# Performance work log

Hardware: AMD Instinct MI355X
Metric: run time of the kernel (lower is better)

## Reference

```python
import jax, jax.numpy as jnp
import numpy as np

BN_EPS = 1e-5


def _gcn_norm(edge_index, n):
    # PyG gcn_norm with add_self_loops=True: deg counts in-degree incl. self loop
    loops = jnp.arange(n, dtype=edge_index.dtype)
    src = jnp.concatenate([edge_index[0], loops])
    dst = jnp.concatenate([edge_index[1], loops])
    deg = jax.ops.segment_sum(jnp.ones(src.shape[0], jnp.float32), dst, num_segments=n)
    dinv = jnp.where(deg > 0, jax.lax.rsqrt(jnp.maximum(deg, 1.0)), 0.0)
    norm = dinv[src] * dinv[dst]  # [E + N]
    return src, dst, norm


def _gcn_conv(x, src, dst, norm, W, b, n):
    h = x @ W                      # dense transform first (fewer FLOPs: d_out gather)
    msgs = h[src] * norm[:, None]  # [E+N, d_out] gathered, degree-normalized
    return jax.ops.segment_sum(msgs, dst, num_segments=n) + b


def _bn_relu(x, gamma, beta):
    # BatchNorm1d in training mode: biased batch stats over node dim
    mu = x.mean(axis=0)
    var = x.var(axis=0)
    return jax.nn.relu(gamma * (x - mu) * jax.lax.rsqrt(var + BN_EPS) + beta)


def setup_inputs() -> dict:
    key = jax.random.key(0)
    ks = jax.random.split(key, 8)
    N, E, D_IN, H1, H2, D_OUT = 50000, 500000, 128, 256, 512, 128
    x = jax.random.normal(ks[0], (N, D_IN), jnp.float32)
    edge_index = jax.random.randint(ks[1], (2, E), 0, N, jnp.int64)
    def lin(k, fan_in, fan_out):
        bound = 1.0 / np.sqrt(fan_in)
        kw, kb = jax.random.split(k)
        W = jax.random.uniform(kw, (fan_in, fan_out), jnp.float32, -bound, bound)
        b = jax.random.uniform(kb, (fan_out,), jnp.float32, -bound, bound)
        return W, b
    W1, b1 = lin(ks[2], D_IN, H1)
    W2, b2 = lin(ks[3], H1, H2)
    Wl, bl = lin(ks[4], H2, D_OUT)
    return {
        "x": x, "edge_index": edge_index,
        "W1": W1, "b1": b1, "gamma1": jnp.ones((H1,), jnp.float32), "beta1": jnp.zeros((H1,), jnp.float32),
        "W2": W2, "b2": b2, "gamma2": jnp.ones((H2,), jnp.float32), "beta2": jnp.zeros((H2,), jnp.float32),
        "Wl": Wl, "bl": bl,
    }


def reference(x, edge_index, W1, b1, gamma1, beta1, W2, b2, gamma2, beta2, Wl, bl):
    n = x.shape[0]
    src, dst, norm = _gcn_norm(edge_index, n)
    h = _bn_relu(_gcn_conv(x, src, dst, norm, W1, b1, n), gamma1, beta1)
    h = _bn_relu(_gcn_conv(h, src, dst, norm, W2, b2, n), gamma2, beta2)
    return h @ Wl + bl
```

## Files before the change

### kernel.cpp

```cpp
#include <hip/hip_runtime.h>
#include <cstdint>
#include <cstddef>

typedef __bf16 bf16;
typedef bf16 bf16x2 __attribute__((ext_vector_type(2)));
typedef bf16 bf16x4 __attribute__((ext_vector_type(4)));
typedef bf16 bf16x8 __attribute__((ext_vector_type(8)));
typedef float f32x4 __attribute__((ext_vector_type(4)));

__global__ void k_init(int* __restrict__ deg, int* __restrict__ cur,
                       float* __restrict__ sums1, float* __restrict__ sums2, int N) {
  int i = blockIdx.x * 256 + threadIdx.x;
  if (i < N) { deg[i] = 1; cur[i] = 0; }
  if (i < 512)  sums1[i] = 0.f;
  if (i < 1024) sums2[i] = 0.f;
}

__global__ void k_count(const int* __restrict__ ei, int* __restrict__ deg, int E) {
  int e = blockIdx.x * 256 + threadIdx.x;
  if (e < E) atomicAdd(&deg[ei[E + e]], 1);
}

__global__ __launch_bounds__(256) void k_scan1(const int* __restrict__ deg,
                                               int* __restrict__ bsum, int N) {
  int t = threadIdx.x;
  int i = blockIdx.x * 256 + t;
  int v = (i < N) ? deg[i] - 1 : 0;
#pragma unroll
  for (int off = 32; off > 0; off >>= 1) v += __shfl_down(v, off, 64);
  __shared__ int red[4];
  if ((t & 63) == 0) red[t >> 6] = v;
  __syncthreads();
  if (t == 0) bsum[blockIdx.x] = red[0] + red[1] + red[2] + red[3];
}

__global__ __launch_bounds__(256) void k_scan2(const int* __restrict__ bsum,
                                               int* __restrict__ bpre, int B) {
  __shared__ int s[256];
  int t = threadIdx.x;
  int v = (t < B) ? bsum[t] : 0;
  s[t] = v;
  __syncthreads();
  for (int off = 1; off < 256; off <<= 1) {
    int add = (t >= off) ? s[t - off] : 0;
    __syncthreads();
    s[t] += add;
    __syncthreads();
  }
  if (t < B) bpre[t] = s[t] - v;
}

__global__ __launch_bounds__(256) void k_scan3(const int* __restrict__ deg,
                                               const int* __restrict__ bpre,
                                               int* __restrict__ roff,
                                               float* __restrict__ dinv, int N) {
  __shared__ int s[256];
  int t = threadIdx.x;
  int i = blockIdx.x * 256 + t;
  int d = (i < N) ? deg[i] : 1;
  int v = d - 1;
  if (i >= N) v = 0;
  s[t] = v;
  __syncthreads();
  for (int off = 1; off < 256; off <<= 1) {
    int add = (t >= off) ? s[t - off] : 0;
    __syncthreads();
    s[t] += add;
    __syncthreads();
  }
  if (i < N) {
    int base = bpre[blockIdx.x];
    roff[i] = base + s[t] - v;
    dinv[i] = rsqrtf((float)d);
    if (i == N - 1) roff[N] = base + s[t];
  }
}

__global__ void k_scatter(const int* __restrict__ ei, const int* __restrict__ roff,
                          int* __restrict__ cur, int* __restrict__ csr, int E) {
  int e = blockIdx.x * 256 + threadIdx.x;
  if (e >= E) return;
  int d = ei[E + e];
  int p = atomicAdd(&cur[d], 1);
  csr[roff[d] + p] = ei[e];
}

__global__ void k_cvt_x(const float* __restrict__ x, bf16* __restrict__ xb, size_t total) {
  size_t base = ((size_t)blockIdx.x * 256 + threadIdx.x) * 4;
  if (base >= total) return;
  const float4 v = *(const float4*)(x + base);
  bf16x4 o;
  o[0] = (bf16)v.x; o[1] = (bf16)v.y; o[2] = (bf16)v.z; o[3] = (bf16)v.w;
  *(bf16x4*)(xb + base) = o;
}

__global__ void k_cvt_w(const float* __restrict__ W1, const float* __restrict__ W2,
                        const float* __restrict__ Wl, bf16* __restrict__ w1t,
                        bf16* __restrict__ w2t, bf16* __restrict__ wlt) {
  int i = blockIdx.x * 256 + threadIdx.x;
  if (i < 32768) {
    int n = i >> 7, k = i & 127;
    w1t[i] = (bf16)W1[(size_t)k * 256 + n];
  } else if (i < 163840) {
    int j = i - 32768;
    int n = j >> 8, k = j & 255;
    w2t[j] = (bf16)W2[(size_t)k * 512 + n];
  } else {
    int j = i - 163840;
    int n = j >> 9, k = j & 511;
    wlt[j] = (bf16)Wl[(size_t)k * 128 + n];
  }
}

template<int K, int NOUT, bool FINAL>
__global__ __launch_bounds__(256) void k_gemm(const bf16* __restrict__ A,
                                              const bf16* __restrict__ Bt,
                                              bf16* __restrict__ outB,
                                              float* __restrict__ outF,
                                              const float* __restrict__ bias,
                                              float* __restrict__ sums,
                                              int Mreal) {
  constexpr int MT  = FINAL ? 64 : 128;
  constexpr int RPW = MT / 32;
  __shared__ uint4 lA[2][MT * 4];
  __shared__ uint4 lB[2][512];
  const int tid = threadIdx.x;
  const int wv = tid >> 6, lane = tid & 63;
  const int q = lane >> 4, mr = lane & 15;
  const int m0 = blockIdx.x * MT;
  const int n0 = blockIdx.y * 128;
  const int rw = (wv >> 1) * (MT / 2), cw = (wv & 1) * 64;

  const int r0 = tid >> 2, j0 = tid & 3;
  const bf16* gA0 = A + (size_t)(m0 + (MT == 64 ? r0 : r0)) * K + j0 * 8;
  const bf16* gA1 = A + (size_t)(m0 + 64 + r0) * K + j0 * 8;
  const bf16* gB0 = Bt + (size_t)(n0 + r0) * K + j0 * 8;
  const bf16* gB1 = Bt + (size_t)(n0 + 64 + r0) * K + j0 * 8;
  const int swz = j0 << 1;
  const int slA0 = j0 * MT + (r0 ^ swz);
  const int slA1 = j0 * MT + ((r0 + 64) ^ swz);
  const int slB0 = j0 * 128 + (r0 ^ swz);
  const int slB1 = j0 * 128 + ((r0 + 64) ^ swz);

  f32x4 acc[RPW][4];
#pragma unroll
  for (int r = 0; r < RPW; ++r)
#pragma unroll
    for (int c = 0; c < 4; ++c) acc[r][c] = (f32x4){0.f, 0.f, 0.f, 0.f};

  uint4 pA0 = *(const uint4*)(gA0);
  uint4 pA1, pB1;
  if constexpr (MT == 128) pA1 = *(const uint4*)(gA1);
  uint4 pB0 = *(const uint4*)(gB0);
  pB1 = *(const uint4*)(gB1);

  const int qs = q << 1;
  int buf = 0;
  for (int k0 = 0; k0 < K; k0 += 32, buf ^= 1) {
    uint4 nA0 = pA0, nA1 = pA1, nB0 = pB0, nB1 = pB1;
    if (k0 + 32 < K) {
      nA0 = *(const uint4*)(gA0 + k0 + 32);
      if constexpr (MT == 128) nA1 = *(const uint4*)(gA1 + k0 + 32);
      nB0 = *(const uint4*)(gB0 + k0 + 32);
      nB1 = *(const uint4*)(gB1 + k0 + 32);
    }
    lA[buf][slA0] = pA0;
    if constexpr (MT == 128) lA[buf][slA1] = pA1;
    lB[buf][slB0] = pB0;
    lB[buf][slB1] = pB1;
    __syncthreads();
    bf16x8 af[RPW], bfr[4];
#pragma unroll
    for (int r = 0; r < RPW; ++r)
      af[r] = ((const bf16x8*)lA[buf])[q * MT + ((rw + r * 16 + mr) ^ qs)];
#pragma unroll
    for (int c = 0; c < 4; ++c)
      bfr[c] = ((const bf16x8*)lB[buf])[q * 128 + ((cw + c * 16 + mr) ^ qs)];
#pragma unroll
    for (int r = 0; r < RPW; ++r)
#pragma unroll
      for (int c = 0; c < 4; ++c)
        acc[r][c] = __builtin_amdgcn_mfma_f32_16x16x32_bf16(af[r], bfr[c], acc[r][c], 0, 0, 0);
    pA0 = nA0; pA1 = nA1; pB0 = nB0; pB1 = nB1;
  }

#pragma unroll
  for (int c = 0; c < 4; ++c) {
    const int col = n0 + cw + c * 16 + mr;
    float s0 = 0.f, s1 = 0.f;
#pragma unroll
    for (int r = 0; r < RPW; ++r) {
#pragma unroll
      for (int i = 0; i < 4; ++i) {
        int row = m0 + rw + r * 16 + q * 4 + i;
        float v = acc[r][c][i];
        if (FINAL) {
          if (row < Mreal) outF[(size_t)row * NOUT + col] = v + bias[col];
        } else {
          outB[(size_t)row * NOUT + col] = (bf16)v;
          if (row < Mreal) { s0 += v; s1 += v * v; }
        }
      }
    }
    if (!FINAL) {
      s0 += __shfl_xor(s0, 16, 64); s0 += __shfl_xor(s0, 32, 64);
      s1 += __shfl_xor(s1, 16, 64); s1 += __shfl_xor(s1, 32, 64);
      if (q == 0) { atomicAdd(&sums[col], s0); atomicAdd(&sums[NOUT + col], s1); }
    }
  }
}

template<int C, bool BN>
__global__ __launch_bounds__(256) void k_agg(const bf16* __restrict__ h,
                                             bf16* __restrict__ g,
                                             const int* __restrict__ csr,
                                             const int* __restrict__ roff,
                                             const float* __restrict__ dinv,
                                             const float* __restrict__ scale,
                                             const float* __restrict__ shift,
                                             int N) {
  constexpr int VPL = C / 64;
  const int lane = threadIdx.x & 63;
  const int v = (int)(((unsigned)blockIdx.x * 256 + threadIdx.x) >> 6);
  if (v >= N) return;
  float sc[VPL], sh[VPL];
  if constexpr (BN) {
#pragma unroll
    for (int u = 0; u < VPL; ++u) { sc[u] = scale[lane * VPL + u]; sh[u] = shift[lane * VPL + u]; }
  }
  const float dv = dinv[v];
  float acc[VPL];
#pragma unroll
  for (int u = 0; u < VPL; ++u) acc[u] = 0.f;

  auto accum = [&](int src, float w) {
    const bf16* hr = h + (size_t)src * C + lane * VPL;
    float vals[VPL];
    if constexpr (VPL == 2) {
      bf16x2 t = *(const bf16x2*)hr;
      vals[0] = (float)t[0]; vals[1] = (float)t[1];
    } else {
      bf16x4 t = *(const bf16x4*)hr;
#pragma unroll
      for (int u = 0; u < 4; ++u) vals[u] = (float)t[u];
    }
#pragma unroll
    for (int u = 0; u < VPL; ++u) {
      float xx = vals[u];
      if constexpr (BN) xx = fmaxf(0.f, xx * sc[u] + sh[u]);
      acc[u] += w * xx;
    }
  };

  accum(v, dv);
  const int beg = roff[v], end = roff[v + 1];
  for (int base = beg; base < end; base += 64) {
    int cnt = min(64, end - base);
    int s = 0; float w = 0.f;
    if (lane < cnt) { s = csr[base + lane]; w = dinv[s]; }
    for (int j = 0; j < cnt; ++j) {
      int sj = __shfl(s, j, 64);
      float wj = __shfl(w, j, 64);
      accum(sj, wj);
    }
  }

  bf16* gv = g + (size_t)v * C + lane * VPL;
  if constexpr (VPL == 2) {
    bf16x2 o;
    o[0] = (bf16)(acc[0] * dv); o[1] = (bf16)(acc[1] * dv);
    *(bf16x2*)gv = o;
  } else {
    bf16x4 o;
#pragma unroll
    for (int u = 0; u < 4; ++u) o[u] = (bf16)(acc[u] * dv);
    *(bf16x4*)gv = o;
  }
}

__global__ void k_bnfinal(const float* __restrict__ sums, const float* __restrict__ gamma,
                          const float* __restrict__ beta, float* __restrict__ scale,
                          float* __restrict__ shift, int C, float invN) {
  int c = blockIdx.x * 256 + threadIdx.x;
  if (c >= C) return;
  float mu = sums[c] * invN;
  float var = sums[C + c] * invN - mu * mu;
  float is = rsqrtf(var + 1e-5f);
  float sc = gamma[c] * is;
  scale[c] = sc;
  shift[c] = beta[c] - mu * sc;
}

template<int C>
__global__ void k_bnapply(bf16* __restrict__ g, const float* __restrict__ scale,
                          const float* __restrict__ shift, size_t total) {
  size_t base = ((size_t)blockIdx.x * 256 + threadIdx.x) * 8;
  if (base >= total) return;
  int col = (int)(base & (size_t)(C - 1));
  bf16x8 t = *(const bf16x8*)(g + base);
  bf16x8 o;
#pragma unroll
  for (int j = 0; j < 8; ++j)
    o[j] = (bf16)fmaxf(0.f, (float)t[j] * scale[col + j] + shift[col + j]);
  *(bf16x8*)(g + base) = o;
}

extern "C" void kernel_launch(void* const* d_in, const int* in_sizes, int n_in,
                              void* d_out, int out_size, void* d_ws, size_t ws_size,
                              hipStream_t stream) {
  const float* x   = (const float*)d_in[0];
  const int*   ei  = (const int*)d_in[1];
  const float* W1  = (const float*)d_in[2];
  const float* g1  = (const float*)d_in[4];
  const float* be1 = (const float*)d_in[5];
  const float* W2  = (const float*)d_in[6];
  const float* g2  = (const float*)d_in[8];
  const float* be2 = (const float*)d_in[9];
  const float* Wl  = (const float*)d_in[10];
  const float* bl  = (const float*)d_in[11];
  float* out = (float*)d_out;

  const int N  = in_sizes[0] / 128;
  const int E  = in_sizes[1] / 2;
  const int Mp = ((N + 127) / 128) * 128;
  const int NB = (N + 255) / 256;

  char* p = (char*)d_ws;
  auto carve = [&](size_t bytes) { void* r = (void*)p; p += (bytes + 255) & ~(size_t)255; return r; };
  int*   deg   = (int*)carve(sizeof(int) * N);
  int*   cur   = (int*)carve(sizeof(int) * N);
  int*   roff  = (int*)carve(sizeof(int) * (N + 1));
  int*   csr   = (int*)carve(sizeof(int) * E);
  int*   bsum  = (int*)carve(sizeof(int) * 256);
  int*   bpre  = (int*)carve(sizeof(int) * 256);
  float* dinv  = (float*)carve(sizeof(float) * N);
  float* sums1 = (float*)carve(sizeof(float) * 512);
  float* sums2 = (float*)carve(sizeof(float) * 1024);
  float* sc1   = (float*)carve(sizeof(float) * 256);
  float* sh1   = (float*)carve(sizeof(float) * 256);
  float* sc2   = (float*)carve(sizeof(float) * 512);
  float* sh2   = (float*)carve(sizeof(float) * 512);
  bf16*  w1t   = (bf16*)carve(sizeof(bf16) * 256 * 128);
  bf16*  w2t   = (bf16*)carve(sizeof(bf16) * 512 * 256);
  bf16*  wlt   = (bf16*)carve(sizeof(bf16) * 128 * 512);
  bf16*  xb    = (bf16*)carve(sizeof(bf16) * (size_t)Mp * 128);
  bf16*  ax1   = (bf16*)carve(sizeof(bf16) * (size_t)Mp * 128);
  bf16*  t1    = (bf16*)carve(sizeof(bf16) * (size_t)Mp * 256);
  bf16*  ax2   = (bf16*)carve(sizeof(bf16) * (size_t)Mp * 256);
  bf16*  t2    = (bf16*)carve(sizeof(bf16) * (size_t)Mp * 512);
  (void)n_in; (void)out_size; (void)ws_size;

  const int gE = (E + 255) / 256;
  k_init<<<NB, 256, 0, stream>>>(deg, cur, sums1, sums2, N);
  k_count<<<gE, 256, 0, stream>>>(ei, deg, E);
  k_scan1<<<NB, 256, 0, stream>>>(deg, bsum, N);
  k_scan2<<<1, 256, 0, stream>>>(bsum, bpre, NB);
  k_scan3<<<NB, 256, 0, stream>>>(deg, bpre, roff, dinv, N);
  k_scatter<<<gE, 256, 0, stream>>>(ei, roff, cur, csr, E);

  k_cvt_x<<<(int)(((size_t)N * 128 / 4 + 255) / 256), 256, 0, stream>>>(x, xb, (size_t)N * 128);
  k_cvt_w<<<896, 256, 0, stream>>>(W1, W2, Wl, w1t, w2t, wlt);

  const int gAgg = (N + 3) / 4;
  k_agg<128, false><<<gAgg, 256, 0, stream>>>(xb, ax1, csr, roff, dinv, nullptr, nullptr, N);
  k_gemm<128, 256, false><<<dim3(Mp / 128, 2), 256, 0, stream>>>(ax1, w1t, t1, nullptr, nullptr, sums1, N);
  k_bnfinal<<<1, 256, 0, stream>>>(sums1, g1, be1, sc1, sh1, 256, 1.f / (float)N);

  k_agg<256, true><<<gAgg, 256, 0, stream>>>(t1, ax2, csr, roff, dinv, sc1, sh1, N);
  k_gemm<256, 512, false><<<dim3(Mp / 128, 4), 256, 0, stream>>>(ax2, w2t, t2, nullptr, nullptr, sums2, N);
  k_bnfinal<<<2, 256, 0, stream>>>(sums2, g2, be2, sc2, sh2, 512, 1.f / (float)N);
  k_bnapply<512><<<(int)(((size_t)Mp * 512 / 8 + 255) / 256), 256, 0, stream>>>(t2, sc2, sh2, (size_t)Mp * 512);

  k_gemm<512, 128, true><<<dim3(Mp / 64, 1), 256, 0, stream>>>(t2, wlt, nullptr, out, bl, nullptr, N);
}
```

Baseline: 382.9 us.

## Fuse BN2+ReLU into final GEMM A-load and deepen GEMM prefetch to two stages

New measurement: 425.9 us. 11.2% more time.

```diff
diff --git a/kernel.cpp b/kernel.cpp
--- a/kernel.cpp
+++ b/kernel.cpp
@@ -119,9 +119,12 @@
                                               float* __restrict__ outF,
                                               const float* __restrict__ bias,
                                               float* __restrict__ sums,
+                                              const float* __restrict__ bnsc,
+                                              const float* __restrict__ bnsh,
                                               int Mreal) {
   constexpr int MT  = FINAL ? 64 : 128;
   constexpr int RPW = MT / 32;
+  constexpr int NIT = K / 32;
   __shared__ uint4 lA[2][MT * 4];
   __shared__ uint4 lB[2][512];
   const int tid = threadIdx.x;
@@ -132,7 +135,7 @@
   const int rw = (wv >> 1) * (MT / 2), cw = (wv & 1) * 64;
 
   const int r0 = tid >> 2, j0 = tid & 3;
-  const bf16* gA0 = A + (size_t)(m0 + (MT == 64 ? r0 : r0)) * K + j0 * 8;
+  const bf16* gA0 = A + (size_t)(m0 + r0) * K + j0 * 8;
   const bf16* gA1 = A + (size_t)(m0 + 64 + r0) * K + j0 * 8;
   const bf16* gB0 = Bt + (size_t)(n0 + r0) * K + j0 * 8;
   const bf16* gB1 = Bt + (size_t)(n0 + 64 + r0) * K + j0 * 8;
@@ -148,40 +151,70 @@
 #pragma unroll
     for (int c = 0; c < 4; ++c) acc[r][c] = (f32x4){0.f, 0.f, 0.f, 0.f};
 
-  uint4 pA0 = *(const uint4*)(gA0);
-  uint4 pA1, pB1;
-  if constexpr (MT == 128) pA1 = *(const uint4*)(gA1);
-  uint4 pB0 = *(const uint4*)(gB0);
-  pB1 = *(const uint4*)(gB1);
+  uint4 qA0[2], qA1[2], qB0[2], qB1[2];
+  float4 qsc[2][2], qsh[2][2];
+#pragma unroll
+  for (int t = 0; t < 2; ++t) {
+    qA0[t] = *(const uint4*)(gA0 + t * 32);
+    if constexpr (MT == 128) qA1[t] = *(const uint4*)(gA1 + t * 32);
+    qB0[t] = *(const uint4*)(gB0 + t * 32);
+    qB1[t] = *(const uint4*)(gB1 + t * 32);
+    if constexpr (FINAL) {
+      int cb = t * 32 + j0 * 8;
+      qsc[t][0] = *(const float4*)(bnsc + cb);
+      qsc[t][1] = *(const float4*)(bnsc + cb + 4);
+      qsh[t][0] = *(const float4*)(bnsh + cb);
+      qsh[t][1] = *(const float4*)(bnsh + cb + 4);
+    }
+  }
 
   const int qs = q << 1;
-  int buf = 0;
-  for (int k0 = 0; k0 < K; k0 += 32, buf ^= 1) {
-    uint4 nA0 = pA0, nA1 = pA1, nB0 = pB0, nB1 = pB1;
-    if (k0 + 32 < K) {
-      nA0 = *(const uint4*)(gA0 + k0 + 32);
-      if constexpr (MT == 128) nA1 = *(const uint4*)(gA1 + k0 + 32);
-      nB0 = *(const uint4*)(gB0 + k0 + 32);
-      nB1 = *(const uint4*)(gB1 + k0 + 32);
-    }
-    lA[buf][slA0] = pA0;
-    if constexpr (MT == 128) lA[buf][slA1] = pA1;
-    lB[buf][slB0] = pB0;
-    lB[buf][slB1] = pB1;
-    __syncthreads();
+#pragma unroll
+  for (int i = 0; i < NIT; ++i) {
+    const int sl = i & 1;
+    uint4 wA0 = qA0[sl];
+    if constexpr (FINAL) {
+      bf16x8 a = *(bf16x8*)&wA0;
+      float s[8] = {qsc[sl][0].x, qsc[sl][0].y, qsc[sl][0].z, qsc[sl][0].w,
+                    qsc[sl][1].x, qsc[sl][1].y, qsc[sl][1].z, qsc[sl][1].w};
+      float h[8] = {qsh[sl][0].x, qsh[sl][0].y, qsh[sl][0].z, qsh[sl][0].w,
+                    qsh[sl][1].x, qsh[sl][1].y, qsh[sl][1].z, qsh[sl][1].w};
+#pragma unroll
+      for (int u = 0; u < 8; ++u)
+        a[u] = (bf16)fmaxf(0.f, (float)a[u] * s[u] + h[u]);
+      wA0 = *(uint4*)&a;
+    }
+    lA[sl][slA0] = wA0;
+    if constexpr (MT == 128) lA[sl][slA1] = qA1[sl];
+    lB[sl][slB0] = qB0[sl];
+    lB[sl][slB1] = qB1[sl];
+    __syncthreads();
+    if (i + 2 < NIT) {
+      int kn = (i + 2) * 32;
+      qA0[sl] = *(const uint4*)(gA0 + kn);
+      if constexpr (MT == 128) qA1[sl] = *(const uint4*)(gA1 + kn);
+      qB0[sl] = *(const uint4*)(gB0 + kn);
+      qB1[sl] = *(const uint4*)(gB1 + kn);
+      if constexpr (FINAL) {
+        int cb = kn + j0 * 8;
+        qsc[sl][0] = *(const float4*)(bnsc + cb);
+        qsc[sl][1] = *(const float4*)(bnsc + cb + 4);
+        qsh[sl][0] = *(const float4*)(bnsh + cb);
+        qsh[sl][1] = *(const float4*)(bnsh + cb + 4);
+      }
+    }
     bf16x8 af[RPW], bfr[4];
 #pragma unroll
     for (int r = 0; r < RPW; ++r)
-      af[r] = ((const bf16x8*)lA[buf])[q * MT + ((rw + r * 16 + mr) ^ qs)];
+      af[r] = ((const bf16x8*)lA[sl])[q * MT + ((rw + r * 16 + mr) ^ qs)];
 #pragma unroll
     for (int c = 0; c < 4; ++c)
-      bfr[c] = ((const bf16x8*)lB[buf])[q * 128 + ((cw + c * 16 + mr) ^ qs)];
+      bfr[c] = ((const bf16x8*)lB[sl])[q * 128 + ((cw + c * 16 + mr) ^ qs)];
 #pragma unroll
     for (int r = 0; r < RPW; ++r)
 #pragma unroll
       for (int c = 0; c < 4; ++c)
         acc[r][c] = __builtin_amdgcn_mfma_f32_16x16x32_bf16(af[r], bfr[c], acc[r][c], 0, 0, 0);
-    pA0 = nA0; pA1 = nA1; pB0 = nB0; pB1 = nB1;
   }
 
 #pragma unroll
@@ -289,20 +322,6 @@
   float sc = gamma[c] * is;
   scale[c] = sc;
   shift[c] = beta[c] - mu * sc;
-}
-
-template<int C>
-__global__ void k_bnapply(bf16* __restrict__ g, const float* __restrict__ scale,
-                          const float* __restrict__ shift, size_t total) {
-  size_t base = ((size_t)blockIdx.x * 256 + threadIdx.x) * 8;
-  if (base >= total) return;
-  int col = (int)(base & (size_t)(C - 1));
-  bf16x8 t = *(const bf16x8*)(g + base);
-  bf16x8 o;
-#pragma unroll
-  for (int j = 0; j < 8; ++j)
-    o[j] = (bf16)fmaxf(0.f, (float)t[j] * scale[col + j] + shift[col + j]);
-  *(bf16x8*)(g + base) = o;
 }
 
 extern "C" void kernel_launch(void* const* d_in, const int* in_sizes, int n_in,
@@ -363,13 +382,12 @@
 
   const int gAgg = (N + 3) / 4;
   k_agg<128, false><<<gAgg, 256, 0, stream>>>(xb, ax1, csr, roff, dinv, nullptr, nullptr, N);
-  k_gemm<128, 256, false><<<dim3(Mp / 128, 2), 256, 0, stream>>>(ax1, w1t, t1, nullptr, nullptr, sums1, N);
+  k_gemm<128, 256, false><<<dim3(Mp / 128, 2), 256, 0, stream>>>(ax1, w1t, t1, nullptr, nullptr, sums1, nullptr, nullptr, N);
   k_bnfinal<<<1, 256, 0, stream>>>(sums1, g1, be1, sc1, sh1, 256, 1.f / (float)N);
 
   k_agg<256, true><<<gAgg, 256, 0, stream>>>(t1, ax2, csr, roff, dinv, sc1, sh1, N);
-  k_gemm<256, 512, false><<<dim3(Mp / 128, 4), 256, 0, stream>>>(ax2, w2t, t2, nullptr, nullptr, sums2, N);
+  k_gemm<256, 512, false><<<dim3(Mp / 128, 4), 256, 0, stream>>>(ax2, w2t, t2, nullptr, nullptr, sums2, nullptr, nullptr, N);
   k_bnfinal<<<2, 256, 0, stream>>>(sums2, g2, be2, sc2, sh2, 512, 1.f / (float)N);
-  k_bnapply<512><<<(int)(((size_t)Mp * 512 / 8 + 255) / 256), 256, 0, stream>>>(t2, sc2, sh2, (size_t)Mp * 512);
-
-  k_gemm<512, 128, true><<<dim3(Mp / 64, 1), 256, 0, stream>>>(t2, wlt, nullptr, out, bl, nullptr, N);
-}
+
+  k_gemm<512, 128, true><<<dim3(Mp / 64, 1), 256, 0, stream>>>(t2, wlt, nullptr, out, bl, nullptr, sc2, sh2, N);
+}
```
